# Performance work log

Hardware: AMD Instinct MI355X
Metric: run time of the kernel (lower is better)

The kernel has to match this reference:

```python
import jax, jax.numpy as jnp
import numpy as np
import math

D_MODEL = 1024
N_HEADS = 16
D_HEAD = D_MODEL // N_HEADS
D_FF = 4096
BATCH = 2
SEQ = 2048
EPS = 1e-5


def _rmsnorm(x, w):
    rms = jnp.sqrt(jnp.mean(x * x, axis=-1, keepdims=True) + EPS)
    return (x / rms) * w


def _gelu_erf(x):
    # matches 0.5 * x * (1 + erf(x / sqrt(2)))
    return 0.5 * x * (1.0 + jax.lax.erf(x / jnp.sqrt(jnp.asarray(2.0, x.dtype))))


def setup_inputs() -> dict:
    key = jax.random.key(0)
    ks = jax.random.split(key, 6)
    scale = 0.02
    x = jax.random.normal(ks[0], (BATCH, SEQ, D_MODEL), dtype=jnp.float32)
    w_qkv = jax.random.normal(ks[1], (3 * D_MODEL, D_MODEL), dtype=jnp.float32) * scale
    w_o = jax.random.normal(ks[2], (D_MODEL, D_MODEL), dtype=jnp.float32) * scale
    ln1_w = jnp.ones((D_MODEL,), dtype=jnp.float32)
    ln2_w = jnp.ones((D_MODEL,), dtype=jnp.float32)
    w1 = jax.random.normal(ks[3], (D_FF, D_MODEL), dtype=jnp.float32) * scale
    w2 = jax.random.normal(ks[4], (D_MODEL, D_FF), dtype=jnp.float32) * scale
    return {"x": x, "w_qkv": w_qkv, "w_o": w_o, "ln1_w": ln1_w,
            "ln2_w": ln2_w, "w1": w1, "w2": w2}


def reference(x, w_qkv, w_o, ln1_w, ln2_w, w1, w2):
    B, S, D = x.shape
    # --- attention sublayer (pre-norm) ---
    h = _rmsnorm(x, ln1_w)
    qkv = jnp.einsum('bsd,ed->bse', h, w_qkv)            # (B,S,3*D)
    qkv = qkv.reshape(B, S, 3, N_HEADS, D_HEAD)
    q, k, v = jnp.moveaxis(qkv, 2, 0)                    # each (B,S,H,dh)
    q = q.transpose(0, 2, 1, 3)                          # (B,H,S,dh)
    k = k.transpose(0, 2, 1, 3)
    v = v.transpose(0, 2, 1, 3)
    scores = jnp.einsum('bhqd,bhkd->bhqk', q, k) / math.sqrt(D_HEAD)
    causal = jnp.tril(jnp.ones((S, S), dtype=bool))      # True = keep
    scores = jnp.where(causal, scores, jnp.asarray(-jnp.inf, scores.dtype))
    attn = jax.nn.softmax(scores, axis=-1)
    ctx = jnp.einsum('bhqk,bhkd->bhqd', attn, v)         # (B,H,S,dh)
    ctx = ctx.transpose(0, 2, 1, 3).reshape(B, S, D)
    attn_out = jnp.einsum('bsd,ed->bse', ctx, w_o)
    first_sum = x + attn_out
    # --- FFN sublayer (pre-norm) ---
    h2 = _rmsnorm(first_sum, ln2_w)
    ff = jnp.einsum('bsf,df->bsd', _gelu_erf(jnp.einsum('bsd,fd->bsf', h2, w1)), w2)
    return first_sum + ff
```

## Files before the change

kernel.cpp:

```cpp
#include <hip/hip_runtime.h>

typedef unsigned short u16;
typedef unsigned int u32;
typedef __attribute__((ext_vector_type(8))) short short8;
typedef __attribute__((ext_vector_type(4))) float f32x4;

#define AS1 __attribute__((address_space(1)))
#define AS3 __attribute__((address_space(3)))

__device__ __forceinline__ u16 f2bf(float f) {
  union { float f; unsigned u; } v; v.f = f;
  return (u16)((v.u + 0x7fffu + ((v.u >> 16) & 1u)) >> 16);
}
__device__ __forceinline__ u32 pack2bf(float a, float b) {
  return (u32)f2bf(a) | ((u32)f2bf(b) << 16);
}
__device__ __forceinline__ float bf2f(u16 h) {
  union { u32 u; float f; } v; v.u = ((u32)h) << 16; return v.f;
}
__device__ __forceinline__ u32 permpack(float a, float b) {
  union { float f; u32 u; } ua, ub; ua.f = a; ub.f = b;
  return __builtin_amdgcn_perm(ub.u, ua.u, 0x07060302u);
}

__global__ __launch_bounds__(256)
void packb_kernel(const float* __restrict__ wqkv, const float* __restrict__ wo,
                  const float* __restrict__ w1, const float* __restrict__ w2,
                  u16* __restrict__ oqkv, u16* __restrict__ oo,
                  u16* __restrict__ o1, u16* __restrict__ o2) {
  __shared__ u16 Ls[128][40];
  const int b = blockIdx.x, t = threadIdx.x;
  const float* W; u16* O; int nb, kb, KB; float scale = 1.0f;
  if (b < 768)       { W = wqkv; O = oqkv; KB = 32;  int i2 = b;        nb = i2 >> 5; kb = i2 & 31;
                       if (nb >= 8 && nb < 16) scale = 0.125f; }
  else if (b < 1024) { W = wo;   O = oo;   KB = 32;  int i2 = b - 768;  nb = i2 >> 5; kb = i2 & 31; }
  else if (b < 2048) { W = w1;   O = o1;   KB = 32;  int i2 = b - 1024; nb = i2 >> 5; kb = i2 & 31; }
  else               { W = w2;   O = o2;   KB = 128; int i2 = b - 2048; nb = i2 >> 7; kb = i2 & 127; }
  const int K = KB * 32;
  {
    const int r = t >> 1, c0 = (t & 1) * 16;
    const float* src = W + (size_t)(nb * 128 + r) * K + kb * 32 + c0;
#pragma unroll
    for (int e = 0; e < 16; ++e) Ls[r][c0 + e] = f2bf(src[e] * scale);
  }
  __syncthreads();
  const int f = t >> 5, l0 = (t & 31) * 2;
  u16* dst = O + ((size_t)(nb * KB + kb) * 8 + f) * 512 + (size_t)l0 * 8;
  short8 v0, v1;
#pragma unroll
  for (int e = 0; e < 8; ++e) v0[e] = (short)Ls[f * 16 + (l0 & 15)][(l0 >> 4) * 8 + e];
  const int l1 = l0 + 1;
#pragma unroll
  for (int e = 0; e < 8; ++e) v1[e] = (short)Ls[f * 16 + (l1 & 15)][(l1 >> 4) * 8 + e];
  *(short8*)dst = v0;
  *(short8*)(dst + 8) = v1;
}

__global__ void rmsnorm_kernel(const float* __restrict__ x, const float* __restrict__ w,
                               u16* __restrict__ out) {
  const int row = blockIdx.x, tid = threadIdx.x;
  const float4 v = ((const float4*)(x + (size_t)row * 1024))[tid];
  float ss = v.x * v.x + v.y * v.y + v.z * v.z + v.w * v.w;
#pragma unroll
  for (int off = 32; off > 0; off >>= 1) ss += __shfl_xor(ss, off);
  __shared__ float red[4];
  if ((tid & 63) == 0) red[tid >> 6] = ss;
  __syncthreads();
  float tot = red[0] + red[1] + red[2] + red[3];
  float scale = 1.0f / sqrtf(tot * (1.0f / 1024.0f) + 1e-5f);
  const float4 wv = ((const float4*)w)[tid];
  ushort4 o = make_ushort4(f2bf(v.x * scale * wv.x), f2bf(v.y * scale * wv.y),
                           f2bf(v.z * scale * wv.z), f2bf(v.w * scale * wv.w));
  ((ushort4*)(out + (size_t)row * 1024))[tid] = o;
}

template <int EPI>
__global__ __launch_bounds__(256, 3)
void gemm_bt(const u16* __restrict__ A, const u16* __restrict__ Bp,
             const float* __restrict__ RES, void* __restrict__ OUT,
             int M, int N, int K, int KS) {
  __shared__ __align__(16) u16 As[2][128 * 32];
  const int tid = threadIdx.x;
  const int wave = tid >> 6, lane = tid & 63;
  const int quad = lane >> 4, l16 = lane & 15;

  int bx = blockIdx.x, by = blockIdx.y;
  const int gx = gridDim.x, gy = gridDim.y;
  if (((gx & 1) | (gy & 3)) == 0) {
    const int lin = blockIdx.x + gx * blockIdx.y;
    const int xcd = lin & 7, j = lin >> 3;
    const int rw = gx >> 1;
    bx = (xcd & 1) * rw + j % rw;
    by = (xcd >> 1) * (gy >> 2) + j / rw;
  }
  const int m0 = by * 128;
  const int wm = (wave >> 1) * 64, wn = (wave & 1) * 64;
  f32x4 acc[4][4] = {};

  const int c0 = wave * 128 + lane;
  const int r0_row = c0 >> 2, r0_col = (c0 & 3) * 8;
  const int c1 = c0 + 64;
  const int r1_row = c1 >> 2, r1_col = (c1 & 3) * 8;
  const u16* ga0 = A + (size_t)(m0 + r0_row) * K + r0_col;
  const u16* ga1 = A + (size_t)(m0 + r1_row) * K + r1_col;

  const u16* Bw = Bp + (((size_t)bx * (K >> 5)) * 8 + (wave & 1) * 4) * 512
                  + (size_t)lane * 8;

  const int kbeg = blockIdx.z * KS, kend = kbeg + KS;

  auto stage = [&](int k0, int pp) {
    __builtin_amdgcn_global_load_lds((AS1 void*)(ga0 + k0), (AS3 void*)(&As[pp][wave * 1024]), 16, 0, 0);
    __builtin_amdgcn_global_load_lds((AS1 void*)(ga1 + k0), (AS3 void*)(&As[pp][wave * 1024 + 512]), 16, 0, 0);
  };

  stage(kbeg, 0);
  short8 bfr[4];
  {
    const u16* bp = Bw + (size_t)(kbeg >> 5) * 4096;
#pragma unroll
    for (int j = 0; j < 4; ++j) bfr[j] = *(const short8*)(bp + j * 512);
  }
  int p = 0;
  for (int k0 = kbeg; k0 < kend - 32; k0 += 32) {
    __syncthreads();
    stage(k0 + 32, p ^ 1);
    short8 bnext[4];
    {
      const u16* bp = Bw + (size_t)((k0 + 32) >> 5) * 4096;
#pragma unroll
      for (int j = 0; j < 4; ++j) bnext[j] = *(const short8*)(bp + j * 512);
    }
    short8 af[4];
#pragma unroll
    for (int i = 0; i < 4; ++i)
      af[i] = *(const short8*)(&As[p][(wm + i * 16 + l16) * 32 + quad * 8]);
#pragma unroll
    for (int i = 0; i < 4; ++i)
#pragma unroll
      for (int j = 0; j < 4; ++j)
        acc[i][j] = __builtin_amdgcn_mfma_f32_16x16x32_bf16(af[i], bfr[j], acc[i][j], 0, 0, 0);
#pragma unroll
    for (int j = 0; j < 4; ++j) bfr[j] = bnext[j];
    p ^= 1;
  }
  {
    __syncthreads();
    short8 af[4];
#pragma unroll
    for (int i = 0; i < 4; ++i)
      af[i] = *(const short8*)(&As[p][(wm + i * 16 + l16) * 32 + quad * 8]);
#pragma unroll
    for (int i = 0; i < 4; ++i)
#pragma unroll
      for (int j = 0; j < 4; ++j)
        acc[i][j] = __builtin_amdgcn_mfma_f32_16x16x32_bf16(af[i], bfr[j], acc[i][j], 0, 0, 0);
  }

  const int n0 = bx * 128;
  const size_t zoff = (size_t)blockIdx.z * M * N;
#pragma unroll
  for (int i = 0; i < 4; ++i) {
#pragma unroll
    for (int j = 0; j < 4; ++j) {
#pragma unroll
      for (int r = 0; r < 4; ++r) {
        int row = m0 + wm + i * 16 + quad * 4 + r;
        int col = n0 + wn + j * 16 + l16;
        size_t idx = (size_t)row * N + col;
        float v = acc[i][j][r];
        if constexpr (EPI == 0) {
          ((u16*)OUT)[idx] = f2bf(v);
        } else if constexpr (EPI == 1) {
          ((float*)OUT)[idx] = RES[idx] + v;
        } else if constexpr (EPI == 2) {
          float g = 0.5f * v * (1.0f + erff(v * 0.70710678118654752f));
          ((u16*)OUT)[idx] = f2bf(g);
        } else {
          ((u16*)OUT)[zoff + idx] = f2bf(v);
        }
      }
    }
  }
}

__global__ void reduce4_kernel(const float* __restrict__ fs,
                               const u16* __restrict__ P,
                               float* __restrict__ out, size_t n) {
  size_t i = ((size_t)blockIdx.x * 256 + threadIdx.x) * 4;
  float4 a = *(const float4*)(fs + i);
  float s[4] = {a.x, a.y, a.z, a.w};
#pragma unroll
  for (int z = 0; z < 4; ++z) {
    ushort4 q = *(const ushort4*)(P + z * n + i);
    s[0] += bf2f(q.x); s[1] += bf2f(q.y); s[2] += bf2f(q.z); s[3] += bf2f(q.w);
  }
  *(float4*)(out + i) = make_float4(s[0], s[1], s[2], s[3]);
}

__global__ __launch_bounds__(256)
void packkv_kernel(const u16* __restrict__ qkv, u16* __restrict__ Kp,
                   u16* __restrict__ Vp) {
  __shared__ __align__(16) u16 Ks[32][72];
  __shared__ __align__(16) u16 Vs[32][72];
  const int kt = blockIdx.x, h = blockIdx.y, b = blockIdx.z;
  const int tid = threadIdx.x;
  const int key0 = kt * 32;
  {
    const size_t g = (size_t)b * 2048 * 3072 + (size_t)(key0 + (tid >> 3)) * 3072
                     + h * 64 + (tid & 7) * 8;
    *(short8*)(&Ks[tid >> 3][(tid & 7) * 8]) = *(const short8*)(qkv + g + 1024);
    *(short8*)(&Vs[tid >> 3][(tid & 7) * 8]) = *(const short8*)(qkv + g + 2048);
  }
  __syncthreads();
  const int wave = tid >> 6, lane = tid & 63;
  const int quad = lane >> 4, l16 = lane & 15;
  const int permrow = 8 * (l16 >> 2) + (l16 & 3);
  const size_t obase = ((size_t)((b * 16 + h) * 64 + kt)) * 2048 + tid * 8;
  {
    int row = permrow + (wave >> 1) * 4;
    int col = quad * 8 + (wave & 1) * 32;
    *(short8*)(Kp + obase) = *(const short8*)(&Ks[row][col]);
  }
  {
    short8 v;
    int col = wave * 16 + l16;
#pragma unroll
    for (int j = 0; j < 8; ++j) v[j] = (short)Vs[quad * 8 + j][col];
    *(short8*)(Vp + obase) = v;
  }
}

struct AttnState {
  f32x4 o0, o1, o2, o3;
  float ls;
};

template <bool MASKED>
__device__ __forceinline__ void attn_tile(
    AttnState& st, const u16* kp, const u16* vp, int key0, int q_abs, int quad,
    short8 qf0, short8 qf1) {
  short8 kf00 = *(const short8*)kp;
  short8 kf01 = *(const short8*)(kp + 512);
  short8 kf10 = *(const short8*)(kp + 1024);
  short8 kf11 = *(const short8*)(kp + 1536);
  short8 vf0 = *(const short8*)vp;
  short8 vf1 = *(const short8*)(vp + 512);
  short8 vf2 = *(const short8*)(vp + 1024);
  short8 vf3 = *(const short8*)(vp + 1536);

  f32x4 s0 = {}, s1 = {};
  s0 = __builtin_amdgcn_mfma_f32_16x16x32_bf16(kf00, qf0, s0, 0, 0, 0);
  s0 = __builtin_amdgcn_mfma_f32_16x16x32_bf16(kf01, qf1, s0, 0, 0, 0);
  s1 = __builtin_amdgcn_mfma_f32_16x16x32_bf16(kf10, qf0, s1, 0, 0, 0);
  s1 = __builtin_amdgcn_mfma_f32_16x16x32_bf16(kf11, qf1, s1, 0, 0, 0);

  float p[8];
#pragma unroll
  for (int r = 0; r < 4; ++r) {
    p[r]     = __expf(s0[r]);
    p[4 + r] = __expf(s1[r]);
  }
  if constexpr (MASKED) {
    const int kb = key0 + 8 * quad;
#pragma unroll
    for (int r = 0; r < 4; ++r) {
      if (kb + r > q_abs)     p[r] = 0.f;
      if (kb + 4 + r > q_abs) p[4 + r] = 0.f;
    }
  }
  st.ls += ((p[0] + p[1]) + (p[2] + p[3])) + ((p[4] + p[5]) + (p[6] + p[7]));

  union { u32 u[4]; short8 s; } pu;
  pu.u[0] = permpack(p[0], p[1]);
  pu.u[1] = permpack(p[2], p[3]);
  pu.u[2] = permpack(p[4], p[5]);
  pu.u[3] = permpack(p[6], p[7]);

  st.o0 = __builtin_amdgcn_mfma_f32_16x16x32_bf16(vf0, pu.s, st.o0, 0, 0, 0);
  st.o1 = __builtin_amdgcn_mfma_f32_16x16x32_bf16(vf1, pu.s, st.o1, 0, 0, 0);
  st.o2 = __builtin_amdgcn_mfma_f32_16x16x32_bf16(vf2, pu.s, st.o2, 0, 0, 0);
  st.o3 = __builtin_amdgcn_mfma_f32_16x16x32_bf16(vf3, pu.s, st.o3, 0, 0, 0);
}

__global__ __launch_bounds__(256)
void attn_kernel(const u16* __restrict__ qkv, const u16* __restrict__ Kpack,
                 const u16* __restrict__ Vpack, u16* __restrict__ ctx) {
  const int bx = blockIdx.x, by = blockIdx.y, bz = blockIdx.z;
  const int h = by, b = bz;
  const int qt = ((by >> 3) & 1) ? (31 - bx) : bx;
  const int tid = threadIdx.x, wave = tid >> 6, lane = tid & 63;
  const int quad = lane >> 4, l16 = lane & 15;
  const int q0 = qt * 64;
  const int qrow = q0 + wave * 16;
  const int q_abs = qrow + l16;
  const size_t base = (size_t)b * 2048 * 3072;
  const size_t headoff = (size_t)((b * 16 + h) * 64) * 2048;
  const u16* Kb = Kpack + headoff + lane * 8;
  const u16* Vb = Vpack + headoff + lane * 8;

  short8 qf0, qf1;
  {
    const u16* qp = qkv + base + (size_t)q_abs * 3072 + h * 64 + quad * 8;
    qf0 = *(const short8*)qp;
    qf1 = *(const short8*)(qp + 32);
  }
  AttnState st;
  st.o0 = f32x4{}; st.o1 = f32x4{}; st.o2 = f32x4{}; st.o3 = f32x4{};
  st.ls = 0.f;

  const int nfull = qrow >> 5;
  for (int kt = 0; kt < nfull; ++kt)
    attn_tile<false>(st, Kb + kt * 2048, Vb + kt * 2048, kt * 32, q_abs, quad, qf0, qf1);
  attn_tile<true>(st, Kb + nfull * 2048, Vb + nfull * 2048, nfull * 32, q_abs, quad, qf0, qf1);

  float ls = st.ls;
  ls += __shfl_xor(ls, 16);
  ls += __shfl_xor(ls, 32);
  float inv = 1.0f / ls;

  f32x4 o[4] = {st.o0, st.o1, st.o2, st.o3};
  u16* cp = ctx + (size_t)(b * 2048 + q_abs) * 1024 + h * 64 + quad * 4;
#pragma unroll
  for (int c = 0; c < 4; ++c) {
    u32 lo = pack2bf(o[c][0] * inv, o[c][1] * inv);
    u32 hi = pack2bf(o[c][2] * inv, o[c][3] * inv);
    *(uint2*)(cp + c * 16) = make_uint2(lo, hi);
  }
}

extern "C" void kernel_launch(void* const* d_in, const int* in_sizes, int n_in,
                              void* d_out, int out_size, void* d_ws, size_t ws_size,
                              hipStream_t stream) {
  const float* x     = (const float*)d_in[0];
  const float* w_qkv = (const float*)d_in[1];
  const float* w_o   = (const float*)d_in[2];
  const float* ln1   = (const float*)d_in[3];
  const float* ln2   = (const float*)d_in[4];
  const float* w1    = (const float*)d_in[5];
  const float* w2    = (const float*)d_in[6];
  float* out = (float*)d_out;

  char* p = (char*)d_ws;
  u16* wqkv_b = (u16*)p; p += (size_t)3072 * 1024 * 2;
  u16* wo_b   = (u16*)p; p += (size_t)1024 * 1024 * 2;
  u16* w1_b   = (u16*)p; p += (size_t)4096 * 1024 * 2;
  u16* w2_b   = (u16*)p; p += (size_t)1024 * 4096 * 2;
  u16* h_b    = (u16*)p; p += (size_t)4096 * 1024 * 2;
  u16* qkv_b  = (u16*)p;
  u16* g_b    = qkv_b;
  p += (size_t)4096 * 3072 * 2;
  u16* ctx_b  = (u16*)p; p += (size_t)4096 * 1024 * 2;
  float* fs   = (float*)p; p += (size_t)4096 * 1024 * 4;
  u16* kp_b   = (u16*)fs;
  u16* vp_b   = (u16*)fs + (size_t)4 * 1024 * 1024;
  u16* Pbuf = (u16*)p;
  const size_t need = (size_t)(p - (char*)d_ws) + (size_t)4 * 4096 * 1024 * 2;
  const bool splitk = ws_size >= need;

  packb_kernel<<<3072, 256, 0, stream>>>(w_qkv, w_o, w1, w2,
                                         wqkv_b, wo_b, w1_b, w2_b);

  rmsnorm_kernel<<<4096, 256, 0, stream>>>(x, ln1, h_b);
  gemm_bt<0><<<dim3(24, 32, 1), 256, 0, stream>>>(h_b, wqkv_b, nullptr, qkv_b, 4096, 3072, 1024, 1024);
  packkv_kernel<<<dim3(64, 16, 2), 256, 0, stream>>>(qkv_b, kp_b, vp_b);
  attn_kernel<<<dim3(32, 16, 2), 256, 0, stream>>>(qkv_b, kp_b, vp_b, ctx_b);
  gemm_bt<1><<<dim3(8, 32, 1), 256, 0, stream>>>(ctx_b, wo_b, x, fs, 4096, 1024, 1024, 1024);
  rmsnorm_kernel<<<4096, 256, 0, stream>>>(fs, ln2, h_b);
  gemm_bt<2><<<dim3(32, 32, 1), 256, 0, stream>>>(h_b, w1_b, nullptr, g_b, 4096, 4096, 1024, 1024);
  if (splitk) {
    gemm_bt<3><<<dim3(8, 32, 4), 256, 0, stream>>>(g_b, w2_b, nullptr, Pbuf, 4096, 1024, 4096, 1024);
    reduce4_kernel<<<4096, 256, 0, stream>>>(fs, Pbuf, out, (size_t)4096 * 1024);
  } else {
    gemm_bt<1><<<dim3(8, 32, 1), 256, 0, stream>>>(g_b, w2_b, fs, out, 4096, 1024, 4096, 4096);
  }
}
```

Measured before the change: 321.2 us.

## Pre-pack GEMM A operands into MFMA fragment layout and drop LDS staging

The producers of GEMM A operands (rmsnorm, attention output, GELU epilogue) now write their bf16 results directly in a packed MFMA-fragment layout. The GEMM then loads both A and B fragments straight from global memory into registers and no longer stages A through LDS with barriers. This removes shared-memory traffic and __syncthreads from the main loop. In exchange, each wave loads its own A fragments, so A is re-read by both N-waves with no LDS sharing, and the GELU epilogue does scattered 2-byte stores.

```diff
diff --git a/kernel.cpp b/kernel.cpp
--- a/kernel.cpp
+++ b/kernel.cpp
@@ -22,6 +22,7 @@
   union { float f; u32 u; } ua, ub; ua.f = a; ub.f = b;
   return __builtin_amdgcn_perm(ub.u, ua.u, 0x07060302u);
 }
+
 
 __global__ __launch_bounds__(256)
 void packb_kernel(const float* __restrict__ wqkv, const float* __restrict__ wo,
@@ -69,21 +70,22 @@
   float tot = red[0] + red[1] + red[2] + red[3];
   float scale = 1.0f / sqrtf(tot * (1.0f / 1024.0f) + 1e-5f);
   const float4 wv = ((const float4*)w)[tid];
-  ushort4 o = make_ushort4(f2bf(v.x * scale * wv.x), f2bf(v.y * scale * wv.y),
-                           f2bf(v.z * scale * wv.z), f2bf(v.w * scale * wv.w));
-  ((ushort4*)(out + (size_t)row * 1024))[tid] = o;
+  const int kb = tid >> 3, quadp = (tid >> 1) & 3, e0 = (tid & 1) * 4;
+  const int mb = row >> 7, i_o = (row >> 4) & 7, l16_o = row & 15;
+  size_t off = (((size_t)mb * 32 + kb) * 8 + i_o) * 512 + (quadp * 16 + l16_o) * 8 + e0;
+  u32 lo = pack2bf(v.x * scale * wv.x, v.y * scale * wv.y);
+  u32 hi = pack2bf(v.z * scale * wv.z, v.w * scale * wv.w);
+  *(uint2*)(out + off) = make_uint2(lo, hi);
 }
 
 template <int EPI>
 __global__ __launch_bounds__(256, 3)
-void gemm_bt(const u16* __restrict__ A, const u16* __restrict__ Bp,
+void gemm_pp(const u16* __restrict__ Ap, const u16* __restrict__ Bp,
              const float* __restrict__ RES, void* __restrict__ OUT,
              int M, int N, int K, int KS) {
-  __shared__ __align__(16) u16 As[2][128 * 32];
   const int tid = threadIdx.x;
   const int wave = tid >> 6, lane = tid & 63;
   const int quad = lane >> 4, l16 = lane & 15;
-
   int bx = blockIdx.x, by = blockIdx.y;
   const int gx = gridDim.x, gy = gridDim.y;
   if (((gx & 1) | (gy & 3)) == 0) {
@@ -93,71 +95,44 @@
     bx = (xcd & 1) * rw + j % rw;
     by = (xcd >> 1) * (gy >> 2) + j / rw;
   }
-  const int m0 = by * 128;
   const int wm = (wave >> 1) * 64, wn = (wave & 1) * 64;
+  const int KB = K >> 5;
   f32x4 acc[4][4] = {};
 
-  const int c0 = wave * 128 + lane;
-  const int r0_row = c0 >> 2, r0_col = (c0 & 3) * 8;
-  const int c1 = c0 + 64;
-  const int r1_row = c1 >> 2, r1_col = (c1 & 3) * 8;
-  const u16* ga0 = A + (size_t)(m0 + r0_row) * K + r0_col;
-  const u16* ga1 = A + (size_t)(m0 + r1_row) * K + r1_col;
-
-  const u16* Bw = Bp + (((size_t)bx * (K >> 5)) * 8 + (wave & 1) * 4) * 512
-                  + (size_t)lane * 8;
-
-  const int kbeg = blockIdx.z * KS, kend = kbeg + KS;
-
-  auto stage = [&](int k0, int pp) {
-    __builtin_amdgcn_global_load_lds((AS1 void*)(ga0 + k0), (AS3 void*)(&As[pp][wave * 1024]), 16, 0, 0);
-    __builtin_amdgcn_global_load_lds((AS1 void*)(ga1 + k0), (AS3 void*)(&As[pp][wave * 1024 + 512]), 16, 0, 0);
-  };
-
-  stage(kbeg, 0);
-  short8 bfr[4];
-  {
-    const u16* bp = Bw + (size_t)(kbeg >> 5) * 4096;
-#pragma unroll
-    for (int j = 0; j < 4; ++j) bfr[j] = *(const short8*)(bp + j * 512);
-  }
-  int p = 0;
-  for (int k0 = kbeg; k0 < kend - 32; k0 += 32) {
-    __syncthreads();
-    stage(k0 + 32, p ^ 1);
-    short8 bnext[4];
-    {
-      const u16* bp = Bw + (size_t)((k0 + 32) >> 5) * 4096;
-#pragma unroll
-      for (int j = 0; j < 4; ++j) bnext[j] = *(const short8*)(bp + j * 512);
+  const int kb0 = (blockIdx.z * KS) >> 5;
+  const int nkb = KS >> 5;
+  const u16* Aw = Ap + (((size_t)by * KB + kb0) * 8 + (wm >> 4)) * 512 + (size_t)lane * 8;
+  const u16* Bw = Bp + (((size_t)bx * KB + kb0) * 8 + (wn >> 4)) * 512 + (size_t)lane * 8;
+
+  short8 af[4], bfc[4];
+#pragma unroll
+  for (int j = 0; j < 4; ++j) {
+    af[j]  = *(const short8*)(Aw + j * 512);
+    bfc[j] = *(const short8*)(Bw + j * 512);
+  }
+  for (int it = 0; it < nkb - 1; ++it) {
+    Aw += 4096; Bw += 4096;
+    short8 an[4], bn[4];
+#pragma unroll
+    for (int j = 0; j < 4; ++j) {
+      an[j] = *(const short8*)(Aw + j * 512);
+      bn[j] = *(const short8*)(Bw + j * 512);
     }
-    short8 af[4];
 #pragma unroll
     for (int i = 0; i < 4; ++i)
-      af[i] = *(const short8*)(&As[p][(wm + i * 16 + l16) * 32 + quad * 8]);
-#pragma unroll
-    for (int i = 0; i < 4; ++i)
 #pragma unroll
       for (int j = 0; j < 4; ++j)
-        acc[i][j] = __builtin_amdgcn_mfma_f32_16x16x32_bf16(af[i], bfr[j], acc[i][j], 0, 0, 0);
-#pragma unroll
-    for (int j = 0; j < 4; ++j) bfr[j] = bnext[j];
-    p ^= 1;
-  }
-  {
-    __syncthreads();
-    short8 af[4];
-#pragma unroll
-    for (int i = 0; i < 4; ++i)
-      af[i] = *(const short8*)(&As[p][(wm + i * 16 + l16) * 32 + quad * 8]);
-#pragma unroll
-    for (int i = 0; i < 4; ++i)
-#pragma unroll
-      for (int j = 0; j < 4; ++j)
-        acc[i][j] = __builtin_amdgcn_mfma_f32_16x16x32_bf16(af[i], bfr[j], acc[i][j], 0, 0, 0);
-  }
-
-  const int n0 = bx * 128;
+        acc[i][j] = __builtin_amdgcn_mfma_f32_16x16x32_bf16(af[i], bfc[j], acc[i][j], 0, 0, 0);
+#pragma unroll
+    for (int j = 0; j < 4; ++j) { af[j] = an[j]; bfc[j] = bn[j]; }
+  }
+#pragma unroll
+  for (int i = 0; i < 4; ++i)
+#pragma unroll
+    for (int j = 0; j < 4; ++j)
+      acc[i][j] = __builtin_amdgcn_mfma_f32_16x16x32_bf16(af[i], bfc[j], acc[i][j], 0, 0, 0);
+
+  const int m0 = by * 128, n0 = bx * 128;
   const size_t zoff = (size_t)blockIdx.z * M * N;
 #pragma unroll
   for (int i = 0; i < 4; ++i) {
@@ -175,7 +150,11 @@
           ((float*)OUT)[idx] = RES[idx] + v;
         } else if constexpr (EPI == 2) {
           float g = 0.5f * v * (1.0f + erff(v * 0.70710678118654752f));
-          ((u16*)OUT)[idx] = f2bf(g);
+          const int kb_o = col >> 5, quadp = (col >> 3) & 3, e = col & 7;
+          const int mb_o = row >> 7, i_o = (row >> 4) & 7, l16_o = row & 15;
+          size_t off = (((size_t)mb_o * (N >> 5) + kb_o) * 8 + i_o) * 512
+                       + (quadp * 16 + l16_o) * 8 + e;
+          ((u16*)OUT)[off] = f2bf(g);
         } else {
           ((u16*)OUT)[zoff + idx] = f2bf(v);
         }
@@ -319,13 +298,17 @@
   ls += __shfl_xor(ls, 32);
   float inv = 1.0f / ls;
 
+  const int rgl = b * 2048 + q_abs;
+  const int mb = rgl >> 7, i_o = (rgl >> 4) & 7;
   f32x4 o[4] = {st.o0, st.o1, st.o2, st.o3};
-  u16* cp = ctx + (size_t)(b * 2048 + q_abs) * 1024 + h * 64 + quad * 4;
 #pragma unroll
   for (int c = 0; c < 4; ++c) {
+    const int c0 = h * 64 + c * 16 + quad * 4;
+    const int kb = c0 >> 5, quadp = (c0 >> 3) & 3, e0 = c0 & 7;
+    size_t off = (((size_t)mb * 32 + kb) * 8 + i_o) * 512 + (quadp * 16 + l16) * 8 + e0;
     u32 lo = pack2bf(o[c][0] * inv, o[c][1] * inv);
     u32 hi = pack2bf(o[c][2] * inv, o[c][3] * inv);
-    *(uint2*)(cp + c * 16) = make_uint2(lo, hi);
+    *(uint2*)(ctx + off) = make_uint2(lo, hi);
   }
 }
 
@@ -362,16 +345,16 @@
                                          wqkv_b, wo_b, w1_b, w2_b);
 
   rmsnorm_kernel<<<4096, 256, 0, stream>>>(x, ln1, h_b);
-  gemm_bt<0><<<dim3(24, 32, 1), 256, 0, stream>>>(h_b, wqkv_b, nullptr, qkv_b, 4096, 3072, 1024, 1024);
+  gemm_pp<0><<<dim3(24, 32, 1), 256, 0, stream>>>(h_b, wqkv_b, nullptr, qkv_b, 4096, 3072, 1024, 1024);
   packkv_kernel<<<dim3(64, 16, 2), 256, 0, stream>>>(qkv_b, kp_b, vp_b);
   attn_kernel<<<dim3(32, 16, 2), 256, 0, stream>>>(qkv_b, kp_b, vp_b, ctx_b);
-  gemm_bt<1><<<dim3(8, 32, 1), 256, 0, stream>>>(ctx_b, wo_b, x, fs, 4096, 1024, 1024, 1024);
+  gemm_pp<1><<<dim3(8, 32, 1), 256, 0, stream>>>(ctx_b, wo_b, x, fs, 4096, 1024, 1024, 1024);
   rmsnorm_kernel<<<4096, 256, 0, stream>>>(fs, ln2, h_b);
-  gemm_bt<2><<<dim3(32, 32, 1), 256, 0, stream>>>(h_b, w1_b, nullptr, g_b, 4096, 4096, 1024, 1024);
+  gemm_pp<2><<<dim3(32, 32, 1), 256, 0, stream>>>(h_b, w1_b, nullptr, g_b, 4096, 4096, 1024, 1024);
   if (splitk) {
-    gemm_bt<3><<<dim3(8, 32, 4), 256, 0, stream>>>(g_b, w2_b, nullptr, Pbuf, 4096, 1024, 4096, 1024);
+    gemm_pp<3><<<dim3(8, 32, 4), 256, 0, stream>>>(g_b, w2_b, nullptr, Pbuf, 4096, 1024, 4096, 1024);
     reduce4_kernel<<<4096, 256, 0, stream>>>(fs, Pbuf, out, (size_t)4096 * 1024);
   } else {
-    gemm_bt<1><<<dim3(8, 32, 1), 256, 0, stream>>>(g_b, w2_b, fs, out, 4096, 1024, 4096, 4096);
-  }
-}
+    gemm_pp<1><<<dim3(8, 32, 1), 256, 0, stream>>>(g_b, w2_b, fs, out, 4096, 1024, 4096, 4096);
+  }
+}
```

Measured after the change: 326.6 us. No clear change (+1.7%).
